# Optimization experiments

Measured on AMD Instinct MI355X. Metric: run time of the kernel, lower is better.

Reference implementation:

```python
import jax, jax.numpy as jnp
import numpy as np

B, N, E = 8, 1024, 256
IN_DIMS, D_MODEL, H = 2, 64, 4
DH = D_MODEL // H  # 16


def _linear_params(key, fan_in, fan_out):
    k1, k2 = jax.random.split(key)
    bound = 1.0 / np.sqrt(fan_in)
    W = jax.random.uniform(k1, (fan_in, fan_out), jnp.float32, -bound, bound)
    b = jax.random.uniform(k2, (fan_out,), jnp.float32, -bound, bound)
    return W, b


def setup_inputs() -> dict:
    key = jax.random.key(0)
    ks = jax.random.split(key, 12)
    x = jax.random.normal(ks[0], (B, N, IN_DIMS), jnp.float32)
    edge_inital = jax.random.normal(ks[1], (B, H, E, DH), jnp.float32)
    C_edge_inital = jax.random.normal(ks[2], (B, H, E, DH), jnp.float32)
    G = jax.random.uniform(ks[3], (B, E, N), jnp.float32)
    C_G = jax.random.uniform(ks[4], (B, E, N), jnp.float32)
    W_emb, b_emb = _linear_params(ks[5], IN_DIMS, D_MODEL)
    W_q, b_q = _linear_params(ks[6], D_MODEL, D_MODEL)
    W_k, b_k = _linear_params(ks[7], D_MODEL, D_MODEL)
    W_eq, b_eq = _linear_params(ks[8], DH, DH)
    W_ek, b_ek = _linear_params(ks[9], DH, DH)
    W_ceq, b_ceq = _linear_params(ks[10], DH, DH)
    W_cek, b_cek = _linear_params(ks[11], DH, DH)
    return dict(x=x, edge_inital=edge_inital, C_edge_inital=C_edge_inital, G=G, C_G=C_G,
                W_emb=W_emb, b_emb=b_emb, W_q=W_q, b_q=b_q, W_k=W_k, b_k=b_k,
                W_eq=W_eq, b_eq=b_eq, W_ek=W_ek, b_ek=b_ek,
                W_ceq=W_ceq, b_ceq=b_ceq, W_cek=W_cek, b_cek=b_cek)


def _split_heads(t):
    # [B, N, D_MODEL] -> [B, H, N, DH]
    b, n, _ = t.shape
    return t.reshape(b, n, H, DH).transpose(0, 2, 1, 3)


def _branch(q, k, edge, Gm, We_q, be_q, We_k, be_k, scale):
    eq = edge @ We_q + be_q          # [B,H,E,DH]
    ek = edge @ We_k + be_k
    div = Gm.sum(axis=1)[:, None, :, None]  # [B,1,N,1]
    gq = q + jnp.einsum('ben,bhec->bhnc', Gm, eq) / div
    gk = k + jnp.einsum('ben,bhec->bhnc', Gm, ek) / div
    scores = jnp.einsum('bhnc,bhmc->bhnm', gq, gk) / scale
    return jax.nn.softmax(scores, axis=-1)


def reference(x, edge_inital, C_edge_inital, G, C_G,
              W_emb, b_emb, W_q, b_q, W_k, b_k,
              W_eq, b_eq, W_ek, b_ek, W_ceq, b_ceq, W_cek, b_cek):
    scale = jnp.sqrt(jnp.float32(D_MODEL))
    emb = x @ W_emb + b_emb                 # [B,N,D]
    q = _split_heads(emb @ W_q + b_q)       # [B,H,N,DH]
    k = _split_heads(emb @ W_k + b_k)
    g_att = _branch(q, k, edge_inital, G, W_eq, b_eq, W_ek, b_ek, scale)
    cg_att = _branch(q, k, C_edge_inital, C_G, W_ceq, b_ceq, W_cek, b_cek, scale)
    return (g_att, cg_att)
```

## Files before the change

kernel.cpp:

```cpp
#include <hip/hip_runtime.h>
#include <math.h>

#define BB     8
#define NN     1024
#define EE     256
#define DMODEL 64
#define HH     4
#define DHH    16

#define WS_Q    0
#define WS_K    524288
#define WS_GQ   1048576
#define WS_GKT  2097152

__global__ __launch_bounds__(256) void qk_kernel(
    const float* __restrict__ x, const float* __restrict__ W_emb,
    const float* __restrict__ b_emb, const float* __restrict__ W_q,
    const float* __restrict__ b_q, const float* __restrict__ W_k,
    const float* __restrict__ b_k, float* __restrict__ ws) {
  __shared__ float semb[4][DMODEL];
  const int tid = threadIdx.x;
  const int p = tid >> 6, d = tid & 63;
  const int pos = blockIdx.x * 4 + p;
  const float x0 = x[pos * 2 + 0];
  const float x1 = x[pos * 2 + 1];
  semb[p][d] = fmaf(x0, W_emb[d], fmaf(x1, W_emb[DMODEL + d], b_emb[d]));
  __syncthreads();
  float accq = b_q[d], acck = b_k[d];
#pragma unroll 8
  for (int e = 0; e < DMODEL; ++e) {
    const float ev = semb[p][e];
    accq = fmaf(ev, W_q[e * DMODEL + d], accq);
    acck = fmaf(ev, W_k[e * DMODEL + d], acck);
  }
  const int b = pos >> 10, n = pos & (NN - 1);
  const int h = d >> 4, c = d & 15;
  const int oidx = ((b * HH + h) * NN + n) * DHH + c;
  ws[WS_Q + oidx] = accq;
  ws[WS_K + oidx] = acck;
}

__global__ __launch_bounds__(256) void gqgk_kernel(
    const float* __restrict__ G, const float* __restrict__ C_G,
    const float* __restrict__ edge, const float* __restrict__ C_edge,
    const float* __restrict__ W_eq, const float* __restrict__ b_eq,
    const float* __restrict__ W_ek, const float* __restrict__ b_ek,
    const float* __restrict__ W_ceq, const float* __restrict__ b_ceq,
    const float* __restrict__ W_cek, const float* __restrict__ b_cek,
    float* __restrict__ ws) {
  __shared__ float seq[EE * 4];
  __shared__ float sek[EE * 4];
  const int sub = blockIdx.x & 15;
  const int mat = blockIdx.x >> 4;
  const int h = mat & 3;
  const int b = (mat >> 2) & 7;
  const int br = mat >> 5;
  const int nchunk = sub >> 2;
  const int c0 = (sub & 3) * 4;
  const int tid = threadIdx.x;
  const int n = (nchunk << 8) + tid;

  const float* __restrict__ Wq = br ? W_ceq : W_eq;
  const float* __restrict__ Wk = br ? W_cek : W_ek;
  const float* __restrict__ bq = br ? b_ceq : b_eq;
  const float* __restrict__ bk = br ? b_cek : b_ek;
  const float* __restrict__ esrc = br ? C_edge : edge;

  {
    float in[16];
    const float4* s4 = (const float4*)(esrc + ((size_t)(b * HH + h) * EE + tid) * 16);
#pragma unroll
    for (int i = 0; i < 4; ++i) {
      const float4 v = s4[i];
      in[4 * i + 0] = v.x; in[4 * i + 1] = v.y;
      in[4 * i + 2] = v.z; in[4 * i + 3] = v.w;
    }
    float aq[4], ak[4];
#pragma unroll
    for (int j = 0; j < 4; ++j) { aq[j] = bq[c0 + j]; ak[j] = bk[c0 + j]; }
#pragma unroll
    for (int cp = 0; cp < 16; ++cp) {
      const float iv = in[cp];
#pragma unroll
      for (int j = 0; j < 4; ++j) {
        aq[j] = fmaf(iv, Wq[cp * 16 + c0 + j], aq[j]);
        ak[j] = fmaf(iv, Wk[cp * 16 + c0 + j], ak[j]);
      }
    }
#pragma unroll
    for (int j = 0; j < 4; ++j) { seq[tid * 4 + j] = aq[j]; sek[tid * 4 + j] = ak[j]; }
  }
  __syncthreads();

  const float* __restrict__ Gm = br ? C_G : G;
  const float* __restrict__ gcol = Gm + (size_t)b * EE * NN + n;
  float accq[4] = {0.f, 0.f, 0.f, 0.f};
  float acck[4] = {0.f, 0.f, 0.f, 0.f};
  float div = 0.f;
#pragma unroll 8
  for (int e = 0; e < EE; ++e) {
    const float g = gcol[e * NN];
    div += g;
#pragma unroll
    for (int c = 0; c < 4; ++c) {
      accq[c] = fmaf(g, seq[e * 4 + c], accq[c]);
      acck[c] = fmaf(g, sek[e * 4 + c], acck[c]);
    }
  }
  const float inv = 1.0f / div;
  const int qidx = ((b * HH + h) * NN + n) * 16 + c0;
  const float* __restrict__ qrow = ws + WS_Q + qidx;
  const float* __restrict__ krow = ws + WS_K + qidx;
  float* __restrict__ gq = ws + WS_GQ + (mat * NN + n) * 16 + c0;
  float* __restrict__ gkT = ws + WS_GKT + mat * 16 * NN + n;
  float4 qo;
  qo.x = qrow[0] + accq[0] * inv;
  qo.y = qrow[1] + accq[1] * inv;
  qo.z = qrow[2] + accq[2] * inv;
  qo.w = qrow[3] + accq[3] * inv;
  *(float4*)gq = qo;
#pragma unroll
  for (int c = 0; c < 4; ++c)
    gkT[(c0 + c) * NN] = krow[c] + acck[c] * inv;
}

__global__ __launch_bounds__(1024) void attn_kernel(
    const float* __restrict__ ws, float* __restrict__ out) {
  __shared__ float skT[16 * NN];
  __shared__ float sgq[64 * 16];
  const int idx = blockIdx.x;
  const int rb = idx & 15;
  const int mat = idx >> 4;
  const float* __restrict__ gkTp = ws + WS_GKT + mat * 16 * NN;
  const float* __restrict__ gqp = ws + WS_GQ + (mat * NN + rb * 64) * 16;
  const int tid = threadIdx.x;
  const float4* __restrict__ src4 = (const float4*)gkTp;
  float4* dst4 = (float4*)skT;
#pragma unroll
  for (int i = 0; i < 4; ++i) dst4[tid + 1024 * i] = src4[tid + 1024 * i];
  if (tid < 256) ((float4*)sgq)[tid] = ((const float4*)gqp)[tid];
  __syncthreads();
  const int wave = tid >> 6, lane = tid & 63;
  const int r0 = wave * 4;
  float s[4][16];
#pragma unroll
  for (int r = 0; r < 4; ++r)
#pragma unroll
    for (int t = 0; t < 16; ++t) s[r][t] = 0.f;

  for (int c = 0; c < 16; ++c) {
    float gkv[16];
#pragma unroll
    for (int t = 0; t < 16; ++t) gkv[t] = skT[c * NN + lane + 64 * t];
#pragma unroll
    for (int r = 0; r < 4; ++r) {
      const float qv = sgq[(r0 + r) * 16 + c];
#pragma unroll
      for (int t = 0; t < 16; ++t) s[r][t] = fmaf(qv, gkv[t], s[r][t]);
    }
  }

#pragma unroll
  for (int r = 0; r < 4; ++r) {
    float m = s[r][0];
#pragma unroll
    for (int t = 1; t < 16; ++t) m = fmaxf(m, s[r][t]);
#pragma unroll
    for (int off = 32; off; off >>= 1) m = fmaxf(m, __shfl_xor(m, off));
    float sum = 0.f;
#pragma unroll
    for (int t = 0; t < 16; ++t) {
      s[r][t] = __expf((s[r][t] - m) * 0.125f);
      sum += s[r][t];
    }
#pragma unroll
    for (int off = 32; off; off >>= 1) sum += __shfl_xor(sum, off);
    const float inv = 1.0f / sum;
    float* __restrict__ orow =
        out + ((size_t)mat * NN + (size_t)(rb * 64 + r0 + r)) * NN;
#pragma unroll
    for (int t = 0; t < 16; ++t) orow[lane + 64 * t] = s[r][t] * inv;
  }
}

extern "C" void kernel_launch(void* const* d_in, const int* in_sizes, int n_in,
                              void* d_out, int out_size, void* d_ws,
                              size_t ws_size, hipStream_t stream) {
  const float* x      = (const float*)d_in[0];
  const float* edge   = (const float*)d_in[1];
  const float* C_edge = (const float*)d_in[2];
  const float* G      = (const float*)d_in[3];
  const float* C_G    = (const float*)d_in[4];
  const float* W_emb  = (const float*)d_in[5];
  const float* b_emb  = (const float*)d_in[6];
  const float* W_q    = (const float*)d_in[7];
  const float* b_q    = (const float*)d_in[8];
  const float* W_k    = (const float*)d_in[9];
  const float* b_k    = (const float*)d_in[10];
  const float* W_eq   = (const float*)d_in[11];
  const float* b_eq   = (const float*)d_in[12];
  const float* W_ek   = (const float*)d_in[13];
  const float* b_ek   = (const float*)d_in[14];
  const float* W_ceq  = (const float*)d_in[15];
  const float* b_ceq  = (const float*)d_in[16];
  const float* W_cek  = (const float*)d_in[17];
  const float* b_cek  = (const float*)d_in[18];
  float* ws = (float*)d_ws;
  float* out = (float*)d_out;

  hipLaunchKernelGGL(qk_kernel, dim3(BB * NN / 4), dim3(256), 0, stream, x,
                     W_emb, b_emb, W_q, b_q, W_k, b_k, ws);
  hipLaunchKernelGGL(gqgk_kernel, dim3(2 * BB * HH * 16), dim3(256), 0, stream,
                     G, C_G, edge, C_edge, W_eq, b_eq, W_ek, b_ek, W_ceq,
                     b_ceq, W_cek, b_cek, ws);
  hipLaunchKernelGGL(attn_kernel, dim3(2 * BB * HH * 16), dim3(1024), 0,
                     stream, ws, out);
}
```

Before: 378.0 us.

## Read gkT directly from global in attention, shrink blocks, vectorize stores

The attention kernel no longer stages the full 64KB transposed gk matrix in shared memory. Each block now handles 16 rows with 256 threads and reads gk as float4 straight from global or L2, and writes the output with float4 stores. This removes the large LDS staging and its occupancy limit and gives four times as many blocks for latency hiding. The cost is redundant global reads of gk across 64 blocks per matrix, which rely on L2 hits.

```diff
diff --git a/kernel.cpp b/kernel.cpp
--- a/kernel.cpp
+++ b/kernel.cpp
@@ -124,39 +124,44 @@
     gkT[(c0 + c) * NN] = krow[c] + acck[c] * inv;
 }
 
-__global__ __launch_bounds__(1024) void attn_kernel(
+__global__ __launch_bounds__(256, 4) void attn_kernel(
     const float* __restrict__ ws, float* __restrict__ out) {
-  __shared__ float skT[16 * NN];
-  __shared__ float sgq[64 * 16];
+  __shared__ float sgq[16 * 16];
   const int idx = blockIdx.x;
-  const int rb = idx & 15;
-  const int mat = idx >> 4;
-  const float* __restrict__ gkTp = ws + WS_GKT + mat * 16 * NN;
-  const float* __restrict__ gqp = ws + WS_GQ + (mat * NN + rb * 64) * 16;
+  const int rb = idx & 63;
+  const int mat = idx >> 6;
+  const float* __restrict__ gkTp = ws + WS_GKT + (size_t)mat * 16 * NN;
+  const float* __restrict__ gqp =
+      ws + WS_GQ + ((size_t)mat * NN + (size_t)rb * 16) * 16;
   const int tid = threadIdx.x;
-  const float4* __restrict__ src4 = (const float4*)gkTp;
-  float4* dst4 = (float4*)skT;
-#pragma unroll
-  for (int i = 0; i < 4; ++i) dst4[tid + 1024 * i] = src4[tid + 1024 * i];
-  if (tid < 256) ((float4*)sgq)[tid] = ((const float4*)gqp)[tid];
+  if (tid < 64) ((float4*)sgq)[tid] = ((const float4*)gqp)[tid];
   __syncthreads();
   const int wave = tid >> 6, lane = tid & 63;
   const int r0 = wave * 4;
+  const int col0 = lane * 4;
+
   float s[4][16];
 #pragma unroll
   for (int r = 0; r < 4; ++r)
 #pragma unroll
     for (int t = 0; t < 16; ++t) s[r][t] = 0.f;
 
+#pragma unroll 4
   for (int c = 0; c < 16; ++c) {
-    float gkv[16];
-#pragma unroll
-    for (int t = 0; t < 16; ++t) gkv[t] = skT[c * NN + lane + 64 * t];
+    float4 g[4];
+#pragma unroll
+    for (int t = 0; t < 4; ++t)
+      g[t] = *(const float4*)(gkTp + c * NN + col0 + 256 * t);
 #pragma unroll
     for (int r = 0; r < 4; ++r) {
       const float qv = sgq[(r0 + r) * 16 + c];
 #pragma unroll
-      for (int t = 0; t < 16; ++t) s[r][t] = fmaf(qv, gkv[t], s[r][t]);
+      for (int t = 0; t < 4; ++t) {
+        s[r][4 * t + 0] = fmaf(qv, g[t].x, s[r][4 * t + 0]);
+        s[r][4 * t + 1] = fmaf(qv, g[t].y, s[r][4 * t + 1]);
+        s[r][4 * t + 2] = fmaf(qv, g[t].z, s[r][4 * t + 2]);
+        s[r][4 * t + 3] = fmaf(qv, g[t].w, s[r][4 * t + 3]);
+      }
     }
   }
 
@@ -177,9 +182,16 @@
     for (int off = 32; off; off >>= 1) sum += __shfl_xor(sum, off);
     const float inv = 1.0f / sum;
     float* __restrict__ orow =
-        out + ((size_t)mat * NN + (size_t)(rb * 64 + r0 + r)) * NN;
-#pragma unroll
-    for (int t = 0; t < 16; ++t) orow[lane + 64 * t] = s[r][t] * inv;
+        out + ((size_t)mat * NN + (size_t)(rb * 16 + r0 + r)) * NN;
+#pragma unroll
+    for (int t = 0; t < 4; ++t) {
+      float4 o;
+      o.x = s[r][4 * t + 0] * inv;
+      o.y = s[r][4 * t + 1] * inv;
+      o.z = s[r][4 * t + 2] * inv;
+      o.w = s[r][4 * t + 3] * inv;
+      *(float4*)(orow + col0 + 256 * t) = o;
+    }
   }
 }
 
@@ -213,6 +225,6 @@
   hipLaunchKernelGGL(gqgk_kernel, dim3(2 * BB * HH * 16), dim3(256), 0, stream,
                      G, C_G, edge, C_edge, W_eq, b_eq, W_ek, b_ek, W_ceq,
                      b_ceq, W_cek, b_cek, ws);
-  hipLaunchKernelGGL(attn_kernel, dim3(2 * BB * HH * 16), dim3(1024), 0,
+  hipLaunchKernelGGL(attn_kernel, dim3(2 * BB * HH * 64), dim3(256), 0,
                      stream, ws, out);
 }
```

Result: no change. 370.9 us (-1.9%).
